# Performance work log

Measured on AMD Instinct MI355X. Metric: run time of the kernel, lower is better.

The kernel has to match this reference:

```python
import jax, jax.numpy as jnp
import numpy as np

B, S, D, H, DK, DFF, L = 4, 1024, 1024, 16, 64, 4096, 128

def setup_inputs() -> dict:
    key = jax.random.key(0)
    ks = jax.random.split(key, 20)
    stdv = 1.0 / np.sqrt(D)
    u = lambda k, shape, s=stdv: jax.random.uniform(k, shape, jnp.float32, -s, s)
    x = jax.random.normal(ks[0], (B, S, D), jnp.float32)
    causal = jnp.triu(jnp.ones((S, S), bool), 1)          # True = masked
    attn_mask = jnp.broadcast_to(causal, (B, S, S))
    return {
        "x": x,
        "attn_mask": attn_mask,
        "W_q": u(ks[1], (H * DK, D)), "b_q": jnp.zeros((H * DK,)),
        "W_k": u(ks[2], (H * DK, D)), "b_k": jnp.zeros((H * DK,)),
        "W_v": u(ks[3], (H * DK, D)), "b_v": jnp.zeros((H * DK,)),
        "W_o": u(ks[4], (D, H * DK)), "b_o": jnp.zeros((D,)),
        "W_rel": u(ks[5], (2 * L + 1, DK), 1.0 / np.sqrt(DK)),
        "ln1_alpha": jnp.ones((D,)), "ln1_bias": jnp.zeros((D,)),
        "ln2_alpha": jnp.ones((D,)), "ln2_bias": jnp.zeros((D,)),
        "W1": u(ks[6], (DFF, D)), "b1": jnp.zeros((DFF,)),
        "W2": u(ks[7], (D, DFF)), "b2": jnp.zeros((D,)),
    }

def _layer_norm(x, alpha, bias, eps=1e-5):
    # Faithful to source: (x - mean) / (std + eps), std is biased (unbiased=False)
    m = jnp.mean(x, axis=-1, keepdims=True)
    std = jnp.sqrt(jnp.mean((x - m) ** 2, axis=-1, keepdims=True))
    return alpha * (x - m) / (std + eps) + bias

def reference(x, attn_mask, W_q, b_q, W_k, b_k, W_v, b_v, W_o, b_o, W_rel,
              ln1_alpha, ln1_bias, ln2_alpha, ln2_bias, W1, b1, W2, b2):
    b, s, d = x.shape
    q = (x @ W_q.T + b_q).reshape(b, s, H, DK)
    k = (x @ W_k.T + b_k).reshape(b, s, H, DK)
    v = (x @ W_v.T + b_v).reshape(b, s, H, DK)
    # relative position bias table lookup -> [s, s, DK]
    idx = jnp.clip(jnp.arange(s)[:, None] - jnp.arange(s)[None, :], -L, L) + L
    pos = W_rel[idx]
    # NOTE: original uses rel_pos_k_emb for BOTH pos_key and pos_value (as in source).
    scores = jnp.einsum('bqnd,bknd->bnqk', q, k) + jnp.einsum('bqnd,qkd->bnqk', q, pos)
    scores = scores / np.sqrt(DK)
    scores = jnp.where(attn_mask[:, None, :, :], jnp.float32(-10000.0), scores)
    attn = jax.nn.softmax(scores, axis=-1)
    out = jnp.einsum('bnqk,bknd->bnqd', attn, v) + jnp.einsum('bnqk,qkd->bnqd', attn, pos)
    out = out.transpose(0, 2, 1, 3).reshape(b, s, H * DK)
    out = out @ W_o.T + b_o
    # post-LN transformer layer: LN(x + attn), then LN(h + FFN(h))
    h = _layer_norm(x + out, ln1_alpha, ln1_bias)
    f = jax.nn.relu(h @ W1.T + b1) @ W2.T + b2
    return _layer_norm(h + f, ln2_alpha, ln2_bias)
```

## Files before the change

kernel.cpp:

```cpp
#include <hip/hip_runtime.h>
#include <cmath>
#include <cstdint>

typedef __bf16 bf16;
typedef __bf16 bf16x8 __attribute__((ext_vector_type(8)));
typedef __bf16 bf16x4 __attribute__((ext_vector_type(4)));
typedef float f32x4 __attribute__((ext_vector_type(4)));

#define CEXP 0.1803368852f

__device__ __forceinline__ void async_ld16(const void* g, void* l) {
  __builtin_amdgcn_global_load_lds(
      (__attribute__((address_space(1))) void*)(uintptr_t)g,
      (__attribute__((address_space(3))) void*)l, 16, 0, 0);
}

__global__ __launch_bounds__(256) void cast_all(
    const float* __restrict__ x,  const float* __restrict__ wq, const float* __restrict__ wk,
    const float* __restrict__ wv, const float* __restrict__ wo, const float* __restrict__ w1,
    const float* __restrict__ w2,
    bf16* xb, bf16* wqb, bf16* wkb, bf16* wvb, bf16* wob, bf16* w1b, bf16* w2b)
{
  int i = blockIdx.x * 256 + threadIdx.x;
  const int M1 = 1 << 20, Q = 1 << 18;
  const float* src; bf16* dst; int off;
  if      (i < M1)            { src = x;  dst = xb;  off = i; }
  else if (i < M1 + Q)        { src = wq; dst = wqb; off = i - M1; }
  else if (i < M1 + 2 * Q)    { src = wk; dst = wkb; off = i - M1 - Q; }
  else if (i < M1 + 3 * Q)    { src = wv; dst = wvb; off = i - M1 - 2 * Q; }
  else if (i < M1 + 4 * Q)    { src = wo; dst = wob; off = i - M1 - 3 * Q; }
  else if (i < 3 * M1)        { src = w1; dst = w1b; off = i - M1 - 4 * Q; }
  else                        { src = w2; dst = w2b; off = i - 3 * M1; }
  float4 v = ((const float4*)src)[off];
  bf16x4 o; o[0]=(bf16)v.x; o[1]=(bf16)v.y; o[2]=(bf16)v.z; o[3]=(bf16)v.w;
  ((bf16x4*)dst)[off] = o;
}

template<int BM>
__device__ __forceinline__ void gemm_core(
    const bf16* __restrict__ A, const bf16* __restrict__ Bm, const float* __restrict__ bias,
    float* __restrict__ outF, bf16* __restrict__ outB,
    const float* __restrict__ residF, const bf16* __restrict__ residB,
    int N, int kld, int kbeg, int kend, int relu, bf16* As, bf16* Bs)
{
  constexpr int MI = BM / 32;
  const int tid  = threadIdx.x;
  const int wave = tid >> 6, lane = tid & 63;
  const int lr = lane & 15, lq = lane >> 4;
  const int bm = blockIdx.x * BM, bn = blockIdx.y * 128;
  const int wm = (wave >> 1) * (BM / 2), wn = (wave & 1) * 64;
  const int srow = lane >> 2, scol = (lane & 3) * 8;

  const f32x4 fz = {0.f, 0.f, 0.f, 0.f};
  f32x4 acc[MI][4];
#pragma unroll
  for (int i = 0; i < MI; i++)
#pragma unroll
    for (int j = 0; j < 4; j++) acc[i][j] = fz;

  auto issue = [&](int k0, int buf) {
    bf16* Ad = As + buf * (BM * 32);
    bf16* Bd = Bs + buf * (128 * 32);
    if (BM == 128) {
#pragma unroll
      for (int cc = 0; cc < 2; ++cc) {
        int c = wave * 2 + cc;
        async_ld16(A + (size_t)(bm + c * 16 + srow) * kld + k0 + scol, Ad + c * 512);
      }
    } else {
      async_ld16(A + (size_t)(bm + wave * 16 + srow) * kld + k0 + scol, Ad + wave * 512);
    }
#pragma unroll
    for (int cc = 0; cc < 2; ++cc) {
      int c = wave * 2 + cc;
      async_ld16(Bm + (size_t)(bn + c * 16 + srow) * kld + k0 + scol, Bd + c * 512);
    }
  };

  const int nit = (kend - kbeg) >> 5;
  issue(kbeg, 0);
  for (int i = 0; i < nit; i++) {
    __syncthreads();
    if (i + 1 < nit) issue(kbeg + (i + 1) * 32, (i + 1) & 1);
    const bf16* Ab = As + (i & 1) * (BM * 32);
    const bf16* Bb = Bs + (i & 1) * (128 * 32);
    bf16x8 af[MI], bfr[4];
#pragma unroll
    for (int mi = 0; mi < MI; mi++) af[mi]  = *(const bf16x8*)(Ab + (wm + mi*16 + lr)*32 + lq*8);
#pragma unroll
    for (int ni = 0; ni < 4; ni++) bfr[ni] = *(const bf16x8*)(Bb + (wn + ni*16 + lr)*32 + lq*8);
#pragma unroll
    for (int mi = 0; mi < MI; mi++)
#pragma unroll
      for (int ni = 0; ni < 4; ni++)
        acc[mi][ni] = __builtin_amdgcn_mfma_f32_16x16x32_bf16(af[mi], bfr[ni], acc[mi][ni], 0, 0, 0);
  }

#pragma unroll
  for (int ni = 0; ni < 4; ni++) {
    int n = bn + wn + ni*16 + lr;
    float bv = bias ? bias[n] : 0.0f;
#pragma unroll
    for (int mi = 0; mi < MI; mi++) {
#pragma unroll
      for (int r = 0; r < 4; r++) {
        int m = bm + wm + mi*16 + lq*4 + r;
        size_t idx = (size_t)m * N + n;
        float v = acc[mi][ni][r] + bv;
        if (relu) v = fmaxf(v, 0.0f);
        if (residF) v += residF[idx];
        if (residB) v += (float)residB[idx];
        if (outF) outF[idx] = v;
        else      outB[idx] = (bf16)v;
      }
    }
  }
}

template<int BM>
__global__ __launch_bounds__(256) void gemm_bt(
    const bf16* A, const bf16* Bm, const float* bias,
    float* outF, bf16* outB, const float* residF, const bf16* residB,
    int N, int K, int relu)
{
  __shared__ bf16 As[2 * BM * 32];
  __shared__ bf16 Bs[2 * 128 * 32];
  gemm_core<BM>(A, Bm, bias, outF, outB, residF, residB, N, K, 0, K, relu, As, Bs);
}

__global__ __launch_bounds__(256) void gemm_splitk(
    const bf16* A, const bf16* Bm, float* part, int N, int kld, int kchunk)
{
  __shared__ bf16 As[2 * 128 * 32];
  __shared__ bf16 Bs[2 * 128 * 32];
  const int z = blockIdx.z;
  gemm_core<128>(A, Bm, nullptr, part + (size_t)z * 4096 * N, nullptr, nullptr, nullptr,
                 N, kld, z * kchunk, (z + 1) * kchunk, 0, As, Bs);
}

__global__ __launch_bounds__(256) void gemm_qkv(
    const bf16* A, const bf16* Bq, const bf16* Bk, const bf16* Bv,
    const float* bq, const float* bk, const float* bv,
    bf16* Oq, bf16* Ok, bf16* Ov, int N, int K)
{
  __shared__ bf16 As[2 * 128 * 32];
  __shared__ bf16 Bs[2 * 128 * 32];
  const bf16* Bm  = blockIdx.z == 0 ? Bq : (blockIdx.z == 1 ? Bk : Bv);
  const float* bi = blockIdx.z == 0 ? bq : (blockIdx.z == 1 ? bk : bv);
  bf16* O         = blockIdx.z == 0 ? Oq : (blockIdx.z == 1 ? Ok : Ov);
  gemm_core<128>(A, Bm, bi, nullptr, O, nullptr, nullptr, N, K, 0, K, 0, As, Bs);
}

__global__ __launch_bounds__(256) void transpose_v(const bf16* __restrict__ V, bf16* __restrict__ Vt) {
  __shared__ bf16 t[64][72];
  const int tid = threadIdx.x;
  const int sblk = blockIdx.x;
  const int bh = blockIdx.y;
  const int b = bh >> 4, h = bh & 15;
  const int sr = tid >> 2, dc = (tid & 3) * 16;
  const bf16* src = V + ((size_t)(b * 1024 + sblk * 64 + sr)) * 1024 + h * 64 + dc;
  bf16x8 r0 = *(const bf16x8*)src;
  bf16x8 r1 = *(const bf16x8*)(src + 8);
  *(bf16x8*)(&t[sr][dc]) = r0;
  *(bf16x8*)(&t[sr][dc + 8]) = r1;
  __syncthreads();
  const int dr = tid >> 2, sc = (tid & 3) * 16;
  bf16 o[16];
#pragma unroll
  for (int j = 0; j < 16; j++) o[j] = t[sc + j][dr];
  bf16* dst = Vt + ((size_t)(bh * 64 + dr)) * 1024 + sblk * 64 + sc;
  *(bf16x8*)dst = *(bf16x8*)&o[0];
  *(bf16x8*)(dst + 8) = *(bf16x8*)&o[8];
}

#define S_LEN 1024
#define ROWSTR 1024

__global__ __launch_bounds__(256) void attn_kernel(
    const bf16* __restrict__ Qg, const bf16* __restrict__ Kg, const bf16* __restrict__ Vt,
    const float* __restrict__ Wrel, bf16* __restrict__ Og)
{
  __shared__ __align__(16) bf16 hist[64][136];
  __shared__ __align__(16) bf16 rel_s[64][132];
  __shared__ __align__(16) bf16 ovl[8704];
  bf16* V_T  = ovl;
  bf16* Pb   = ovl + 4096;
  bf16* Wst  = ovl;
  bf16* Wr_t = ovl;
  float* lbuf = (float*)rel_s;
  float* hbuf = lbuf + 256;

  const int tid = threadIdx.x;
  const int wave = tid >> 6, lane = tid & 63;
  const int lr = lane & 15, lq = lane >> 4;
  const int qblk = 15 - blockIdx.y;
  const int bh = blockIdx.x;
  const int b = bh >> 4, h = bh & 15;
  const int q0 = qblk * 64;
  const int T = qblk + 1;
  const int nearStart = (T > 3) ? T - 3 : 0;
  const size_t rowbase = (size_t)b * S_LEN * ROWSTR + h * 64;
  const size_t vtbase = (size_t)(bh * 64) * 1024;
  const f32x4 fz = {0.f, 0.f, 0.f, 0.f};

  for (int e = tid; e < 2048; e += 256) {
    float4 v = ((const float4*)(Wrel + 8192))[e];
    bf16x4 o; o[0]=(bf16)v.x; o[1]=(bf16)v.y; o[2]=(bf16)v.z; o[3]=(bf16)v.w;
    ((bf16x4*)Wst)[e] = o;
  }
  {
    uint4 z4 = {0u, 0u, 0u, 0u};
    for (int e = tid; e < 1088; e += 256) ((uint4*)hist)[e] = z4;
  }

  bf16x8 qf[4][2];
#pragma unroll
  for (int qt = 0; qt < 4; qt++)
#pragma unroll
    for (int c = 0; c < 2; c++)
      qf[qt][c] = *(const bf16x8*)(Qg + rowbase + (size_t)(q0 + qt*16 + lr) * ROWSTR + c*32 + lq*8);

  bf16x8 wb[2];
#pragma unroll
  for (int c = 0; c < 2; c++)
#pragma unroll
    for (int j = 0; j < 8; j++)
      wb[c][j] = (bf16)Wrel[(size_t)256 * 64 + c*32 + lq*8 + j];

  __syncthreads();

#pragma unroll
  for (int tt = 0; tt < 2; ++tt)
#pragma unroll
    for (int qt = 0; qt < 4; ++qt) {
      f32x4 a = fz;
#pragma unroll
      for (int c = 0; c < 2; c++) {
        bf16x8 wf = *(const bf16x8*)(Wst + (wave*32 + tt*16 + lr) * 64 + c*32 + lq*8);
        a = __builtin_amdgcn_mfma_f32_16x16x32_bf16(wf, qf[qt][c], a, 0, 0, 0);
      }
      bf16x4 pk; pk[0]=(bf16)(a[0]*CEXP); pk[1]=(bf16)(a[1]*CEXP);
                 pk[2]=(bf16)(a[2]*CEXP); pk[3]=(bf16)(a[3]*CEXP);
      *(bf16x4*)(&rel_s[qt*16 + lr][wave*32 + tt*16 + lq*4]) = pk;
    }
  {
    f32x4 a = fz;
#pragma unroll
    for (int c = 0; c < 2; c++)
      a = __builtin_amdgcn_mfma_f32_16x16x32_bf16(wb[c], qf[wave][c], a, 0, 0, 0);
    if (lq == 0) rel_s[wave*16 + lr][128] = (bf16)(a[0]*CEXP);
  }
  __syncthreads();

  float relc[4];
#pragma unroll
  for (int qt = 0; qt < 4; qt++) relc[qt] = (float)rel_s[qt*16 + lr][128];

  float l_p[4] = {0.f,0.f,0.f,0.f}, h_p[4] = {0.f,0.f,0.f,0.f};
  f32x4 acc_o[4];
#pragma unroll
  for (int dt = 0; dt < 4; dt++) acc_o[dt] = fz;

  const int vd1 = tid >> 3;
  const int vj  = (tid & 7) ^ (vd1 & 7);
  const int krow = 16 * wave + lr;

  uint4 va, vb, va2, vb2;
  bf16x8 kf0, kf1, kn0, kn1;
  {
    const bf16* vp = Vt + vtbase + (size_t)vd1 * 1024 + vj * 8;
    va = *(const uint4*)vp; vb = *(const uint4*)(vp + 32 * 1024);
    const bf16* kp = Kg + rowbase + (size_t)krow * ROWSTR + lq*8;
    kf0 = *(const bf16x8*)kp; kf1 = *(const bf16x8*)(kp + 32);
  }

  for (int kt = 0; kt < T; ++kt) {
    const int k0 = kt * 64;

    f32x4 sc[4];
#pragma unroll
    for (int qt = 0; qt < 4; qt++) {
      sc[qt] = __builtin_amdgcn_mfma_f32_16x16x32_bf16(kf0, qf[qt][0], fz, 0, 0, 0);
      sc[qt] = __builtin_amdgcn_mfma_f32_16x16x32_bf16(kf1, qf[qt][1], sc[qt], 0, 0, 0);
    }
    if (kt + 1 < T) {
      const bf16* vp = Vt + vtbase + (size_t)vd1 * 1024 + k0 + 64 + vj * 8;
      va2 = *(const uint4*)vp; vb2 = *(const uint4*)(vp + 32 * 1024);
      const bf16* kp = Kg + rowbase + (size_t)(k0 + 64 + krow) * ROWSTR + lq*8;
      kn0 = *(const bf16x8*)kp; kn1 = *(const bf16x8*)(kp + 32);
    }

    float pw[4][4];
    if (kt < nearStart) {
#pragma unroll
      for (int qt = 0; qt < 4; qt++) {
#pragma unroll
        for (int r = 0; r < 4; r++) pw[qt][r] = exp2f(fmaf(sc[qt][r], CEXP, relc[qt]));
        float s4 = pw[qt][0] + pw[qt][1] + pw[qt][2] + pw[qt][3];
        l_p[qt] += s4; h_p[qt] += s4;
      }
    } else {
#pragma unroll
      for (int qt = 0; qt < 4; qt++) {
        int qg = q0 + qt*16 + lr;
#pragma unroll
        for (int r = 0; r < 4; r++) {
          int kg = k0 + 16*wave + lq*4 + r;
          float p = 0.0f;
          if (kg <= qg) {
            int t = qg - kg; int tc = t > 128 ? 128 : t;
            p = exp2f(fmaf(sc[qt][r], CEXP, (float)rel_s[qt*16 + lr][tc]));
            l_p[qt] += p;
            if (t >= 128) h_p[qt] += p;
            else          hist[qt*16 + lr][t] = (bf16)p;
          }
          pw[qt][r] = p;
        }
      }
    }

    __syncthreads();
    *(uint4*)(V_T + tid * 8) = va;
    *(uint4*)(V_T + (tid + 256) * 8) = vb;
#pragma unroll
    for (int qt = 0; qt < 4; qt++) {
      bf16x4 pk; pk[0]=(bf16)pw[qt][0]; pk[1]=(bf16)pw[qt][1];
                 pk[2]=(bf16)pw[qt][2]; pk[3]=(bf16)pw[qt][3];
      *(bf16x4*)(Pb + (qt*16 + lr) * 72 + 16*wave + lq*4) = pk;
    }
    __syncthreads();

#pragma unroll
    for (int c = 0; c < 2; c++) {
      bf16x8 pf = *(const bf16x8*)(Pb + (16*wave + lr) * 72 + c*32 + lq*8);
#pragma unroll
      for (int dt = 0; dt < 4; dt++) {
        int vd = dt*16 + lr;
        int jx = (c*4 + lq) ^ (vd & 7);
        bf16x8 vf = *(const bf16x8*)(V_T + ((vd << 3) + jx) * 8);
        acc_o[dt] = __builtin_amdgcn_mfma_f32_16x16x32_bf16(pf, vf, acc_o[dt], 0, 0, 0);
      }
    }
    kf0 = kn0; kf1 = kn1; va = va2; vb = vb2;
  }

#pragma unroll
  for (int qt = 0; qt < 4; qt++) {
    l_p[qt] += __shfl_xor(l_p[qt], 16); l_p[qt] += __shfl_xor(l_p[qt], 32);
    h_p[qt] += __shfl_xor(h_p[qt], 16); h_p[qt] += __shfl_xor(h_p[qt], 32);
  }
  __syncthreads();
  if (lq == 0) {
#pragma unroll
    for (int qt = 0; qt < 4; qt++) {
      lbuf[wave*64 + qt*16 + lr] = l_p[qt];
      hbuf[wave*64 + qt*16 + lr] = h_p[qt];
    }
  }
  for (int e = tid; e < 64 * 128; e += 256) {
    int d = e >> 7, t = e & 127;
    Wr_t[d * 136 + t] = (bf16)Wrel[(size_t)(128 + t) * 64 + d];
  }
  __syncthreads();
#pragma unroll
  for (int c = 0; c < 4; c++) {
    bf16x8 hf = *(const bf16x8*)&hist[wave*16 + lr][c*32 + lq*8];
#pragma unroll
    for (int dt = 0; dt < 4; dt++) {
      bf16x8 wf = *(const bf16x8*)(Wr_t + (dt*16 + lr) * 136 + c*32 + lq*8);
      acc_o[dt] = __builtin_amdgcn_mfma_f32_16x16x32_bf16(hf, wf, acc_o[dt], 0, 0, 0);
    }
  }
  float l4[4], h4[4];
#pragma unroll
  for (int r = 0; r < 4; r++) {
    int q = wave*16 + lq*4 + r;
    l4[r] = lbuf[q] + lbuf[64+q] + lbuf[128+q] + lbuf[192+q];
    h4[r] = hbuf[q] + hbuf[64+q] + hbuf[128+q] + hbuf[192+q];
  }
#pragma unroll
  for (int dt = 0; dt < 4; dt++) {
    float wv = Wrel[(size_t)256 * 64 + dt*16 + lr];
#pragma unroll
    for (int r = 0; r < 4; r++) acc_o[dt][r] += h4[r] * wv;
  }
#pragma unroll
  for (int dt = 0; dt < 4; dt++)
#pragma unroll
    for (int r = 0; r < 4; r++) {
      int qg = q0 + wave*16 + lq*4 + r;
      Og[rowbase + (size_t)qg * ROWSTR + dt*16 + lr] = (bf16)(acc_o[dt][r] / l4[r]);
    }
}

__global__ __launch_bounds__(256) void ln_fuse(
    const float* __restrict__ pA, const float* __restrict__ pB,
    const float* __restrict__ bias,
    const float* __restrict__ residF, const bf16* __restrict__ residB,
    const float* __restrict__ alpha, const float* __restrict__ beta,
    float* __restrict__ outF, bf16* __restrict__ outB)
{
  const int row = blockIdx.x, tid = threadIdx.x;
  const int lane = tid & 63, wave = tid >> 6;
  const size_t base = (size_t)row * 1024;
  float4 v = ((const float4*)(pA + base))[tid];
  float4 v2 = ((const float4*)(pB + base))[tid];
  v.x += v2.x; v.y += v2.y; v.z += v2.z; v.w += v2.w;
  float4 bv = ((const float4*)bias)[tid];
  v.x += bv.x; v.y += bv.y; v.z += bv.z; v.w += bv.w;
  if (residF) {
    float4 rv = ((const float4*)(residF + base))[tid];
    v.x += rv.x; v.y += rv.y; v.z += rv.z; v.w += rv.w;
  }
  if (residB) {
    bf16x4 rv = ((const bf16x4*)(residB + base))[tid];
    v.x += (float)rv[0]; v.y += (float)rv[1]; v.z += (float)rv[2]; v.w += (float)rv[3];
  }
  float s  = v.x + v.y + v.z + v.w;
  float ss = v.x*v.x + v.y*v.y + v.z*v.z + v.w*v.w;
#pragma unroll
  for (int off = 32; off; off >>= 1) { s += __shfl_down(s, off); ss += __shfl_down(ss, off); }
  __shared__ float rs[4], rss[4];
  if (lane == 0) { rs[wave] = s; rss[wave] = ss; }
  __syncthreads();
  s  = rs[0] + rs[1] + rs[2] + rs[3];
  ss = rss[0] + rss[1] + rss[2] + rss[3];
  float mean = s * (1.0f / 1024.0f);
  float var  = ss * (1.0f / 1024.0f) - mean * mean;
  float inv  = 1.0f / (sqrtf(fmaxf(var, 0.0f)) + 1e-5f);
  float4 a = ((const float4*)alpha)[tid];
  float4 bb = ((const float4*)beta)[tid];
  float o0 = a.x * (v.x - mean) * inv + bb.x;
  float o1 = a.y * (v.y - mean) * inv + bb.y;
  float o2 = a.z * (v.z - mean) * inv + bb.z;
  float o3 = a.w * (v.w - mean) * inv + bb.w;
  if (outF) { float4 o = {o0, o1, o2, o3}; ((float4*)(outF + base))[tid] = o; }
  if (outB) { bf16x4 o; o[0]=(bf16)o0; o[1]=(bf16)o1; o[2]=(bf16)o2; o[3]=(bf16)o3;
              ((bf16x4*)(outB + base))[tid] = o; }
}

extern "C" void kernel_launch(void* const* d_in, const int* in_sizes, int n_in,
                              void* d_out, int out_size, void* d_ws, size_t ws_size,
                              hipStream_t stream) {
  (void)in_sizes; (void)n_in; (void)out_size; (void)ws_size;
  const int D = 1024, DFF = 4096;

  const float* x    = (const float*)d_in[0];
  const float* Wq   = (const float*)d_in[2];
  const float* bq   = (const float*)d_in[3];
  const float* Wk   = (const float*)d_in[4];
  const float* bk   = (const float*)d_in[5];
  const float* Wv   = (const float*)d_in[6];
  const float* bv   = (const float*)d_in[7];
  const float* Wo   = (const float*)d_in[8];
  const float* bo   = (const float*)d_in[9];
  const float* Wrel = (const float*)d_in[10];
  const float* g1   = (const float*)d_in[11];
  const float* be1  = (const float*)d_in[12];
  const float* g2   = (const float*)d_in[13];
  const float* be2  = (const float*)d_in[14];
  const float* W1   = (const float*)d_in[15];
  const float* b1   = (const float*)d_in[16];
  const float* W2   = (const float*)d_in[17];
  const float* b2   = (const float*)d_in[18];

  char* ws = (char*)d_ws;
  const size_t MB = 1024 * 1024;
  bf16*  xb   = (bf16*)(ws + 0);
  bf16*  Wqb  = (bf16*)(ws + 8  * MB);
  bf16*  Wkb  = (bf16*)(ws + 10 * MB);
  bf16*  Wvb  = (bf16*)(ws + 12 * MB);
  bf16*  Wob  = (bf16*)(ws + 14 * MB);
  bf16*  W1b  = (bf16*)(ws + 16 * MB);
  bf16*  W2b  = (bf16*)(ws + 24 * MB);
  bf16*  Qb   = (bf16*)(ws + 32 * MB);
  bf16*  Kb   = (bf16*)(ws + 40 * MB);
  bf16*  Vb   = (bf16*)(ws + 48 * MB);
  bf16*  Vt   = (bf16*)(ws + 56 * MB);
  bf16*  AOb  = (bf16*)(ws + 48 * MB);
  float* part = (float*)(ws + 64 * MB);
  bf16*  f1   = Qb;
  bf16*  hb   = xb;

  cast_all<<<16384, 256, 0, stream>>>(x, Wq, Wk, Wv, Wo, W1, W2,
                                      xb, Wqb, Wkb, Wvb, Wob, W1b, W2b);

  gemm_qkv<<<dim3(32, 8, 3), 256, 0, stream>>>(xb, Wqb, Wkb, Wvb, bq, bk, bv, Qb, Kb, Vb, D, D);
  transpose_v<<<dim3(16, 64), 256, 0, stream>>>(Vb, Vt);
  attn_kernel<<<dim3(64, 16), 256, 0, stream>>>(Qb, Kb, Vt, Wrel, AOb);
  gemm_splitk<<<dim3(32, 8, 2), 256, 0, stream>>>(AOb, Wob, part, D, D, 512);
  ln_fuse<<<4096, 256, 0, stream>>>(part, part + 4096 * 1024, bo, x, nullptr, g1, be1, nullptr, hb);
  gemm_bt<128><<<dim3(32, 32), 256, 0, stream>>>(hb, W1b, b1, nullptr, f1, nullptr, nullptr, DFF, D, 1);
  gemm_splitk<<<dim3(32, 8, 2), 256, 0, stream>>>(f1, W2b, part, D, DFF, 2048);
  ln_fuse<<<4096, 256, 0, stream>>>(part, part + 4096 * 1024, b2, nullptr, hb, g2, be2, (float*)d_out, nullptr);
}
```

Baseline: 398.7 us.

## Use 256x256-tile 512-thread GEMM with swizzled LDS for FFN1

Replaces the 128x128-tile GEMM for the first FFN matmul (4096x4096x1024) with a new kernel using 256x256 output tiles, 512 threads, BK=64 and double-buffered async global-to-LDS loads. LDS is XOR-swizzled to avoid bank conflicts, and MFMA sections use setprio. This aims to raise arithmetic intensity and cut global traffic per FLOP. The grid shrinks to 256 blocks, roughly one per CU, and the kernel uses 128KB of LDS and many accumulator registers, so occupancy is minimal and it depends on intra-block pipelining.

```diff
diff --git a/kernel.cpp b/kernel.cpp
--- a/kernel.cpp
+++ b/kernel.cpp
@@ -117,17 +117,6 @@
   }
 }
 
-template<int BM>
-__global__ __launch_bounds__(256) void gemm_bt(
-    const bf16* A, const bf16* Bm, const float* bias,
-    float* outF, bf16* outB, const float* residF, const bf16* residB,
-    int N, int K, int relu)
-{
-  __shared__ bf16 As[2 * BM * 32];
-  __shared__ bf16 Bs[2 * 128 * 32];
-  gemm_core<BM>(A, Bm, bias, outF, outB, residF, residB, N, K, 0, K, relu, As, Bs);
-}
-
 __global__ __launch_bounds__(256) void gemm_splitk(
     const bf16* A, const bf16* Bm, float* part, int N, int kld, int kchunk)
 {
@@ -149,6 +138,119 @@
   const float* bi = blockIdx.z == 0 ? bq : (blockIdx.z == 1 ? bk : bv);
   bf16* O         = blockIdx.z == 0 ? Oq : (blockIdx.z == 1 ? Ok : Ov);
   gemm_core<128>(A, Bm, bi, nullptr, O, nullptr, nullptr, N, K, 0, K, 0, As, Bs);
+}
+
+__global__ __launch_bounds__(512) void gemm256(
+    const bf16* __restrict__ A, const bf16* __restrict__ Bm,
+    const float* __restrict__ bias, bf16* __restrict__ outB,
+    int N, int K, int relu)
+{
+  __shared__ __align__(16) bf16 As[2][256 * 64];
+  __shared__ __align__(16) bf16 Bs[2][256 * 64];
+  const int tid  = threadIdx.x;
+  const int wave = tid >> 6, lane = tid & 63;
+  const int lr = lane & 15, lq = lane >> 4;
+  const int bm = blockIdx.x * 256, bn = blockIdx.y * 256;
+  const int wm = (wave >> 2) * 128, wn = (wave & 3) * 64;
+
+  const f32x4 fz = {0.f, 0.f, 0.f, 0.f};
+  f32x4 acc[8][4];
+#pragma unroll
+  for (int i = 0; i < 8; ++i)
+#pragma unroll
+    for (int j = 0; j < 4; ++j) acc[i][j] = fz;
+
+  int srow[4], scol[4];
+#pragma unroll
+  for (int L = 0; L < 4; ++L) {
+    int cidx = L * 512 + wave * 64 + lane;
+    srow[L] = cidx >> 3;
+    scol[L] = ((cidx & 7) ^ (srow[L] & 7)) * 8;
+  }
+
+  auto issue = [&](int kt, int buf) {
+    const int k0 = kt * 64;
+#pragma unroll
+    for (int L = 0; L < 4; ++L)
+      async_ld16(A + (size_t)(bm + srow[L]) * K + k0 + scol[L],
+                 &As[buf][(L * 512 + wave * 64) * 8]);
+#pragma unroll
+    for (int L = 0; L < 4; ++L)
+      async_ld16(Bm + (size_t)(bn + srow[L]) * K + k0 + scol[L],
+                 &Bs[buf][(L * 512 + wave * 64) * 8]);
+  };
+
+  const int NT = K >> 6;
+  issue(0, 0);
+  issue(1, 1);
+  asm volatile("s_waitcnt vmcnt(8)" ::: "memory");
+  __builtin_amdgcn_sched_barrier(0);
+  __builtin_amdgcn_s_barrier();
+
+  for (int t = 0; t < NT; ++t) {
+    const bf16* Ab = As[t & 1];
+    const bf16* Bb = Bs[t & 1];
+#pragma unroll
+    for (int mh = 0; mh < 2; ++mh) {
+      bf16x8 af[4][2];
+#pragma unroll
+      for (int mi = 0; mi < 4; ++mi) {
+        int row = wm + mh * 64 + mi * 16 + lr;
+#pragma unroll
+        for (int ks = 0; ks < 2; ++ks)
+          af[mi][ks] = *(const bf16x8*)(Ab + row * 64 + (((ks * 4 + lq) ^ (lr & 7)) * 8));
+      }
+#pragma unroll
+      for (int nh = 0; nh < 2; ++nh) {
+        bf16x8 bfr[2][2];
+#pragma unroll
+        for (int ni = 0; ni < 2; ++ni) {
+          int row = wn + nh * 32 + ni * 16 + lr;
+#pragma unroll
+          for (int ks = 0; ks < 2; ++ks)
+            bfr[ni][ks] = *(const bf16x8*)(Bb + row * 64 + (((ks * 4 + lq) ^ (lr & 7)) * 8));
+        }
+        __builtin_amdgcn_s_setprio(1);
+#pragma unroll
+        for (int mi = 0; mi < 4; ++mi)
+#pragma unroll
+          for (int ni = 0; ni < 2; ++ni)
+#pragma unroll
+            for (int ks = 0; ks < 2; ++ks)
+              acc[mh * 4 + mi][nh * 2 + ni] = __builtin_amdgcn_mfma_f32_16x16x32_bf16(
+                  af[mi][ks], bfr[ni][ks], acc[mh * 4 + mi][nh * 2 + ni], 0, 0, 0);
+        __builtin_amdgcn_s_setprio(0);
+      }
+    }
+    if (t + 1 == NT) break;
+    asm volatile("s_waitcnt lgkmcnt(0)" ::: "memory");
+    __builtin_amdgcn_sched_barrier(0);
+    __builtin_amdgcn_s_barrier();
+    if (t + 2 < NT) {
+      issue(t + 2, t & 1);
+      asm volatile("s_waitcnt vmcnt(8)" ::: "memory");
+    } else {
+      asm volatile("s_waitcnt vmcnt(0)" ::: "memory");
+    }
+    __builtin_amdgcn_sched_barrier(0);
+    __builtin_amdgcn_s_barrier();
+  }
+
+#pragma unroll
+  for (int mi8 = 0; mi8 < 8; ++mi8) {
+#pragma unroll
+    for (int ni4 = 0; ni4 < 4; ++ni4) {
+      int n = bn + wn + ni4 * 16 + lr;
+      float bv = bias ? bias[n] : 0.0f;
+#pragma unroll
+      for (int r = 0; r < 4; ++r) {
+        int m = bm + wm + mi8 * 16 + lq * 4 + r;
+        float v = acc[mi8][ni4][r] + bv;
+        if (relu) v = fmaxf(v, 0.0f);
+        outB[(size_t)m * N + n] = (bf16)v;
+      }
+    }
+  }
 }
 
 __global__ __launch_bounds__(256) void transpose_v(const bf16* __restrict__ V, bf16* __restrict__ Vt) {
@@ -490,7 +592,7 @@
   attn_kernel<<<dim3(64, 16), 256, 0, stream>>>(Qb, Kb, Vt, Wrel, AOb);
   gemm_splitk<<<dim3(32, 8, 2), 256, 0, stream>>>(AOb, Wob, part, D, D, 512);
   ln_fuse<<<4096, 256, 0, stream>>>(part, part + 4096 * 1024, bo, x, nullptr, g1, be1, nullptr, hb);
-  gemm_bt<128><<<dim3(32, 32), 256, 0, stream>>>(hb, W1b, b1, nullptr, f1, nullptr, nullptr, DFF, D, 1);
+  gemm256<<<dim3(16, 16), 512, 0, stream>>>(hb, W1b, b1, f1, DFF, D, 1);
   gemm_splitk<<<dim3(32, 8, 2), 256, 0, stream>>>(f1, W2b, part, D, DFF, 2048);
   ln_fuse<<<4096, 256, 0, stream>>>(part, part + 4096 * 1024, b2, nullptr, hb, g2, be2, (float*)d_out, nullptr);
 }
```

Result: faster. 380.9 us (-4.5%).
